# Optimization experiments

Hardware: AMD Instinct MI355X
Metric: run time of the kernel (lower is better)

Reference implementation:

```python
import jax, jax.numpy as jnp
import numpy as np

SEQ = 128; HID = 2048; NH = 8; NKV = 2; NREP = NH // NKV; HD = 256; FF = 4096
PLD = 256; NLT = 35; NLAYERS = 8; WIN = 512; FULL_LEN = 2048; PAST = 1024
FULL_LAYERS = {5}  # Gemma3 pattern: full attention when (i+1) % 6 == 0
PLE_PROJ_SCALE = HID ** -0.5
PLE_IN_SCALE = 0.7071067811865476  # rsqrt(2)
NEG = -1e9


def _rms(x, w, eps=1e-6):
    return x * jax.lax.rsqrt(jnp.mean(x * x, -1, keepdims=True) + eps) * w


def _vnorm(x, eps=1e-6):
    return x * jax.lax.rsqrt(jnp.mean(x * x, -1, keepdims=True) + eps)


def _rope(x, cos, sin):
    # x: (1, H, S, hd); cos/sin: (1, S, hd)
    c = cos[:, None]; s = sin[:, None]
    h = x.shape[-1] // 2
    x1, x2 = x[..., :h], x[..., h:]
    return x * c + jnp.concatenate([-x2, x1], -1) * s


def _rope_tables(pos, theta):
    inv = 1.0 / (theta ** (np.arange(0, HD, 2, dtype=np.float32) / HD))
    ang = pos[:, None] * inv[None, :]
    emb = np.concatenate([ang, ang], -1)  # (S, HD)
    return jnp.asarray(np.cos(emb), jnp.float32)[None], jnp.asarray(np.sin(emb), jnp.float32)[None]


def setup_inputs() -> dict:
    key = jax.random.key(0)
    ks = iter(jax.random.split(key, 64))
    f = lambda shape, s=0.02: jax.random.normal(next(ks), shape, dtype=jnp.float32) * s
    inp = {}
    inp['hidden_states'] = f((1, SEQ, HID), 1.0)
    inp['per_layer_raw'] = f((1, SEQ, NLT * PLD), 1.0)
    pos = np.arange(PAST, PAST + SEQ, dtype=np.float32)
    inp['cos_s'], inp['sin_s'] = _rope_tables(pos, 10000.0)
    inp['cos_f'], inp['sin_f'] = _rope_tables(pos, 1000000.0)
    i_s = np.arange(SEQ); j_f = np.arange(FULL_LEN); j_s = np.arange(WIN)
    inp['causal_mask_full'] = jnp.asarray(np.where(j_f[None, :] <= PAST + i_s[:, None], 0.0, NEG).astype(np.float32))[None, None]
    inp['causal_mask_sliding'] = jnp.asarray(np.where(j_s[None, :] <= WIN - SEQ + i_s[:, None], 0.0, NEG).astype(np.float32))[None, None]
    ind = np.zeros((FULL_LEN, SEQ), np.float32); ind[PAST + i_s, i_s] = 1.0
    inp['update_indicator'] = jnp.asarray(ind)[None, None]
    inp['K_sliding'] = f((7, NKV, WIN, HD), 1.0); inp['V_sliding'] = f((7, NKV, WIN, HD), 1.0)
    inp['K_full'] = f((1, NKV, FULL_LEN, HD), 1.0); inp['V_full'] = f((1, NKV, FULL_LEN, HD), 1.0)
    # learned parameters (stacked over the 8 layers)
    inp['Wq'] = f((NLAYERS, HID, NH * HD)); inp['Wk'] = f((NLAYERS, HID, NKV * HD))
    inp['Wv'] = f((NLAYERS, HID, NKV * HD)); inp['Wo'] = f((NLAYERS, NH * HD, HID))
    inp['w_in_ln'] = jnp.ones((NLAYERS, HID)); inp['w_q_norm'] = jnp.ones((NLAYERS, HD))
    inp['w_k_norm'] = jnp.ones((NLAYERS, HD)); inp['w_post_attn_ln'] = jnp.ones((NLAYERS, HID))
    inp['w_pre_ff_ln'] = jnp.ones((NLAYERS, HID))
    inp['Wgate'] = f((NLAYERS, HID, FF)); inp['Wup'] = f((NLAYERS, HID, FF)); inp['Wdown'] = f((NLAYERS, FF, HID))
    inp['w_post_ff_ln'] = jnp.ones((NLAYERS, HID))
    inp['Wple_gate'] = f((NLAYERS, HID, PLD)); inp['Wple_proj'] = f((NLAYERS, PLD, HID))
    inp['w_post_ple_ln'] = jnp.ones((NLAYERS, HID))
    inp['layer_scalar'] = jnp.ones((NLAYERS,))
    inp['Wple_model_proj'] = f((HID, NLT * PLD)); inp['w_ple_norm'] = jnp.ones((PLD,))
    return inp


def _forward(hidden_states, per_layer_raw, cos_s, sin_s, cos_f, sin_f,
             causal_mask_full, causal_mask_sliding, update_indicator,
             K_sliding, V_sliding, K_full, V_full,
             Wq, Wk, Wv, Wo, w_in_ln, w_q_norm, w_k_norm, w_post_attn_ln,
             w_pre_ff_ln, Wgate, Wup, Wdown, w_post_ff_ln,
             Wple_gate, Wple_proj, w_post_ple_ln, layer_scalar,
             Wple_model_proj, w_ple_norm):
    S = hidden_states.shape[1]
    # PLE: project hidden, per-layer RMSNorm over pld groups, combine with raw per-layer inputs
    proj = (hidden_states @ Wple_model_proj) * PLE_PROJ_SCALE  # (1,S,NLT*PLD)
    proj = _rms(proj.reshape(S, NLT, PLD), w_ple_norm)
    raw = per_layer_raw.reshape(S, NLT, PLD)
    ple = ((proj + raw) * PLE_IN_SCALE).reshape(1, S, NLT * PLD)

    hs = hidden_states
    Ks, Vs, Kf, Vf = K_sliding, V_sliding, K_full, V_full
    new_ks, new_vs = [], []
    si = 0; fi = 0
    for i in range(NLAYERS):
        is_full = i in FULL_LAYERS
        cos, sin = (cos_f, sin_f) if is_full else (cos_s, sin_s)
        res = hs
        h = _rms(hs, w_in_ln[i])
        # Q/K norm is per (token, head) RMS over head_dim, then RoPE
        q = _rms((h @ Wq[i]).reshape(1, S, NH, HD), w_q_norm[i]).transpose(0, 2, 1, 3)
        q = _rope(q, cos, sin)
        k = _rms((h @ Wk[i]).reshape(1, S, NKV, HD), w_k_norm[i]).transpose(0, 2, 1, 3)
        k = _rope(k, cos, sin)
        v = _vnorm((h @ Wv[i]).reshape(1, S, NKV, HD).transpose(0, 2, 1, 3))
        new_ks.append(k); new_vs.append(v)
        if is_full:
            # matmul-based indicator scatter into the full-attention cache slot
            k_sc = jnp.matmul(update_indicator, k)  # (1,NKV,FULL_LEN,HD)
            v_sc = jnp.matmul(update_indicator, v)
            cm = jnp.sum(update_indicator, -1, keepdims=True)  # (1,1,FULL_LEN,1)
            Kf = Kf.at[fi:fi + 1].set(Kf[fi:fi + 1] * (1.0 - cm) + k_sc)
            Vf = Vf.at[fi:fi + 1].set(Vf[fi:fi + 1] * (1.0 - cm) + v_sc)
            K_attn, V_attn, mask = Kf[fi:fi + 1], Vf[fi:fi + 1], causal_mask_full
            fi += 1
        else:
            # sliding-window shift: drop oldest S, append new K/V
            nk = jnp.concatenate([Ks[si:si + 1, :, S:, :], k], axis=2)
            nv = jnp.concatenate([Vs[si:si + 1, :, S:, :], v], axis=2)
            Ks = Ks.at[si:si + 1].set(nk); Vs = Vs.at[si:si + 1].set(nv)
            K_attn, V_attn, mask = nk, nv, causal_mask_sliding
            si += 1
        Ke = jnp.repeat(K_attn, NREP, axis=1)  # GQA repeat_interleave
        Ve = jnp.repeat(V_attn, NREP, axis=1)
        aw = jax.nn.softmax(jnp.einsum('bhsd,bhld->bhsl', q, Ke) + mask, axis=-1)  # no 1/sqrt(hd), as in source
        attn = jnp.einsum('bhsl,bhld->bhsd', aw, Ve).transpose(0, 2, 1, 3).reshape(1, S, NH * HD)
        hs = res + _rms(attn @ Wo[i], w_post_attn_ln[i])
        res = hs
        h2 = _rms(hs, w_pre_ff_ln[i])
        mlp = (jax.nn.gelu(h2 @ Wgate[i], approximate=True) * (h2 @ Wup[i])) @ Wdown[i]
        hs = res + _rms(mlp, w_post_ff_ln[i])
        res = hs
        pls = ple[:, :, i * PLD:(i + 1) * PLD]
        g = jax.nn.gelu(hs @ Wple_gate[i], approximate=True) * pls
        hs = res + _rms(g @ Wple_proj[i], w_post_ple_ln[i])
        hs = hs * layer_scalar[i]
    return hs, jnp.stack(new_ks), jnp.stack(new_vs)


def reference(hidden_states, per_layer_raw, cos_s, sin_s, cos_f, sin_f,
              causal_mask_full, causal_mask_sliding, update_indicator,
              K_sliding, V_sliding, K_full, V_full,
              Wq, Wk, Wv, Wo, w_in_ln, w_q_norm, w_k_norm, w_post_attn_ln,
              w_pre_ff_ln, Wgate, Wup, Wdown, w_post_ff_ln,
              Wple_gate, Wple_proj, w_post_ple_ln, layer_scalar,
              Wple_model_proj, w_ple_norm):
    return _forward(hidden_states, per_layer_raw, cos_s, sin_s, cos_f, sin_f,
                    causal_mask_full, causal_mask_sliding, update_indicator,
                    K_sliding, V_sliding, K_full, V_full,
                    Wq, Wk, Wv, Wo, w_in_ln, w_q_norm, w_k_norm, w_post_attn_ln,
                    w_pre_ff_ln, Wgate, Wup, Wdown, w_post_ff_ln,
                    Wple_gate, Wple_proj, w_post_ple_ln, layer_scalar,
                    Wple_model_proj, w_ple_norm)
```

## Files before the change

### kernel.cpp

```cpp
#include <hip/hip_runtime.h>
#include <stdint.h>

typedef short s16x8 __attribute__((ext_vector_type(8)));
typedef float f32x4 __attribute__((ext_vector_type(4)));
typedef unsigned short u16;

#define MFMA16(a,b,c) __builtin_amdgcn_mfma_f32_16x16x32_bf16((a),(b),(c),0,0,0)
#define ACAP 1184

__device__ __forceinline__ u16 f2bf(float f) {
  union { float f; unsigned u; } v; v.f = f;
  return (u16)((v.u + 0x7FFFu + ((v.u >> 16) & 1u)) >> 16);
}
__device__ __forceinline__ float bf2f(u16 u) {
  union { float f; unsigned v; } x; x.v = ((unsigned)u) << 16; return x.f;
}

__device__ __forceinline__ float block_sum256(float v, float* lred) {
  #pragma unroll
  for (int d = 32; d >= 1; d >>= 1) v += __shfl_xor(v, d);
  __syncthreads();
  if ((threadIdx.x & 63) == 0) lred[threadIdx.x >> 6] = v;
  __syncthreads();
  return (lred[0] + lred[1]) + (lred[2] + lred[3]);
}

__device__ __forceinline__ float gelu_t(float x) {
  float u = 0.7978845608028654f * (x + 0.044715f * x * x * x);
  return 0.5f * x * (1.0f + tanhf(u));
}

__global__ __launch_bounds__(256) void gemm3_k(
    const u16* __restrict__ Ah, const u16* __restrict__ Al, int lda,
    const float* __restrict__ W0, const float* __restrict__ W1, const float* __restrict__ W2,
    int e0, int e1, int ld0, int ld1, int ld2,
    float* __restrict__ out, int N, int kchunk, int Ktot)
{
  __shared__ float red[4 * 2048];
  const int n0 = blockIdx.x * 16;
  const int split = blockIdx.y;
  const float* W; int ldw, c0;
  if (n0 < e0)      { W = W0; ldw = ld0; c0 = n0; }
  else if (n0 < e1) { W = W1; ldw = ld1; c0 = n0 - e0; }
  else              { W = W2; ldw = ld2; c0 = n0 - e1; }
  const int w = threadIdx.x >> 6, l = threadIdx.x & 63;
  const int lr = l & 15, lh = l >> 4;
  const int wk = kchunk >> 2;
  const int k0 = split * kchunk + w * wk, k1 = k0 + wk;
  const u16* Abh = Ah + (size_t)lr * lda + 8 * lh;
  const u16* Abl = Al + (size_t)lr * lda + 8 * lh;
  const float* Wb = W + (size_t)(8 * lh) * ldw + (c0 + lr);

  f32x4 acc[8];
  #pragma unroll
  for (int i = 0; i < 8; i++) acc[i] = (f32x4){0.f,0.f,0.f,0.f};

  float bc[8];
  #pragma unroll
  for (int jj = 0; jj < 8; jj++) bc[jj] = Wb[(size_t)(k0 + jj) * ldw];

  for (int k = k0; k < k1; k += 32) {
    s16x8 ah[8], al[8];
    #pragma unroll
    for (int mt = 0; mt < 8; mt++) {
      ah[mt] = *(const s16x8*)(Abh + (size_t)(16*mt)*lda + k);
      al[mt] = *(const s16x8*)(Abl + (size_t)(16*mt)*lda + k);
    }
    float bn[8];
    if (k + 32 < k1) {
      #pragma unroll
      for (int jj = 0; jj < 8; jj++) bn[jj] = Wb[(size_t)(k + 32 + jj) * ldw];
    }
    s16x8 bh, bl;
    #pragma unroll
    for (int jj = 0; jj < 8; jj++) {
      union { float f; unsigned u; } wv; wv.f = bc[jj];
      bh[jj] = (short)(wv.u >> 16);
      union { float f; unsigned u; } hf; hf.u = wv.u & 0xFFFF0000u;
      union { float f; unsigned u; } lo; lo.f = wv.f - hf.f;
      bl[jj] = (short)(lo.u >> 16);
    }
    #pragma unroll
    for (int mt = 0; mt < 8; mt++) acc[mt] = MFMA16(ah[mt], bh, acc[mt]);
    #pragma unroll
    for (int mt = 0; mt < 8; mt++) acc[mt] = MFMA16(ah[mt], bl, acc[mt]);
    #pragma unroll
    for (int mt = 0; mt < 8; mt++) acc[mt] = MFMA16(al[mt], bh, acc[mt]);
    if (k + 32 < k1) {
      #pragma unroll
      for (int jj = 0; jj < 8; jj++) bc[jj] = bn[jj];
    }
  }
  #pragma unroll
  for (int mt = 0; mt < 8; mt++)
    #pragma unroll
    for (int r = 0; r < 4; r++)
      red[w * 2048 + (16*mt + 4*lh + r) * 16 + lr] = acc[mt][r];
  __syncthreads();
  const size_t ob = (size_t)split * (128 * (size_t)N) + n0;
  #pragma unroll
  for (int i = 0; i < 8; i++) {
    int e = threadIdx.x + 256 * i;
    int row = e >> 4, c = e & 15;
    float s = (red[e] + red[2048 + e]) + (red[4096 + e] + red[6144 + e]);
    out[ob + (size_t)row * N + c] = s;
  }
}

__global__ __launch_bounds__(256) void init_k(
    const float* __restrict__ hid, const float* __restrict__ w0,
    float* __restrict__ hs, u16* __restrict__ h0b, u16* __restrict__ h0l,
    u16* __restrict__ hbf, u16* __restrict__ hbl)
{
  __shared__ float lred[4];
  int s = blockIdx.x, t = threadIdx.x;
  float x[8]; float ss = 0.f;
  #pragma unroll
  for (int i = 0; i < 8; i++) {
    int j = t + 256 * i;
    float v = hid[(size_t)s * 2048 + j];
    x[i] = v; ss += v * v;
    hs[(size_t)s * 2048 + j] = v;
    u16 hi = f2bf(v);
    h0b[(size_t)s * 2048 + j] = hi;
    h0l[(size_t)s * 2048 + j] = f2bf(v - bf2f(hi));
  }
  ss = block_sum256(ss, lred);
  float rs = rsqrtf(ss * (1.f/2048.f) + 1e-6f);
  #pragma unroll
  for (int i = 0; i < 8; i++) {
    int j = t + 256 * i;
    float xn = x[i] * rs * w0[j];
    u16 hi = f2bf(xn);
    hbf[(size_t)s * 2048 + j] = hi;
    hbl[(size_t)s * 2048 + j] = f2bf(xn - bf2f(hi));
  }
}

__global__ __launch_bounds__(256) void ple_norm_k(
    const float* __restrict__ proj, const float* __restrict__ raw,
    const float* __restrict__ wp, float* __restrict__ ple)
{
  __shared__ float lred[4];
  int b = blockIdx.x;
  int s = b / 35, lt = b % 35, t = threadIdx.x;
  size_t idx = (size_t)s * 8960 + lt * 256 + t;
  float p = proj[idx] * 0.022097086912079612f;
  float ss = block_sum256(p * p, lred);
  float rs = rsqrtf(ss * (1.f/256.f) + 1e-6f);
  ple[idx] = (p * rs * wp[t] + raw[idx]) * 0.7071067811865476f;
}

__global__ __launch_bounds__(256) void fill_kv2_k(
    const float* __restrict__ oK, const float* __restrict__ oV,
    u16* __restrict__ Kh, u16* __restrict__ Kl,
    u16* __restrict__ VTh, u16* __restrict__ VTl,
    int olen, int ooff, int old_ld, int nA)
{
  __shared__ float tile[64][65];
  int b = blockIdx.x, t = threadIdx.x;
  if (b < nA) {
    size_t base = (size_t)b * 4096;
    #pragma unroll
    for (int i = 0; i < 16; i++) {
      size_t e = base + t + 256 * i;
      int kv = (int)(e / ((size_t)olen * 256));
      size_t rem = e - (size_t)kv * olen * 256;
      int j = (int)(rem >> 8), d = (int)(rem & 255);
      float v = oK[((size_t)kv * old_ld + ooff + j) * 256 + d];
      u16 hi = f2bf(v);
      size_t dst = (size_t)kv * (ACAP*256) + (size_t)j * 256 + d;
      Kh[dst] = hi;
      Kl[dst] = f2bf(v - bf2f(hi));
    }
  } else {
    int tb = b - nA;
    int tj = olen >> 6;
    int per_kv = tj * 4;
    int kv = tb / per_kv, rem = tb % per_kv;
    int j0 = (rem % tj) * 64, d0 = (rem / tj) * 64;
    #pragma unroll
    for (int i = 0; i < 16; i++) {
      int e = t + 256 * i;
      int jj = e >> 6, dd = e & 63;
      tile[jj][dd] = oV[((size_t)kv * old_ld + ooff + j0 + jj) * 256 + d0 + dd];
    }
    __syncthreads();
    #pragma unroll
    for (int i = 0; i < 16; i++) {
      int e = t + 256 * i;
      int dd = e >> 6, jj = e & 63;
      float v = tile[jj][dd];
      u16 hi = f2bf(v);
      size_t dst = (size_t)kv * (256*ACAP) + (size_t)(d0 + dd) * ACAP + (j0 + jj);
      VTh[dst] = hi;
      VTl[dst] = f2bf(v - bf2f(hi));
    }
  }
}

__global__ __launch_bounds__(256) void prep_attn_k(
    const float* __restrict__ qkvP, int nsplit,
    const float* __restrict__ wq, const float* __restrict__ wk,
    const float* __restrict__ cosb, const float* __restrict__ sinb,
    u16* __restrict__ qh, u16* __restrict__ ql,
    float* __restrict__ outk, float* __restrict__ outv,
    u16* __restrict__ Kh, u16* __restrict__ Kl,
    u16* __restrict__ VTh, u16* __restrict__ VTl, int jbase)
{
  __shared__ float lred[4];
  __shared__ float xs[256];
  int s = blockIdx.x, t = threadIdx.x;
  const float* base = qkvP + (size_t)s * 3072;
  float c = cosb[s * 256 + t], sn = sinb[s * 256 + t];
  #pragma unroll 1
  for (int h = 0; h < 8; h++) {
    float v = 0.f;
    for (int sp = 0; sp < nsplit; sp++) v += base[(size_t)sp * (128*3072) + h * 256 + t];
    float ss = block_sum256(v * v, lred);
    float rs = rsqrtf(ss * (1.f/256.f) + 1e-6f);
    float xn = v * rs * wq[t];
    xs[t] = xn;
    __syncthreads();
    float pr = xs[t ^ 128];
    float ro = (t < 128) ? -pr : pr;
    float qv = xn * c + ro * sn;
    u16 hi = f2bf(qv);
    qh[((size_t)h * 128 + s) * 256 + t] = hi;
    ql[((size_t)h * 128 + s) * 256 + t] = f2bf(qv - bf2f(hi));
    __syncthreads();
  }
  #pragma unroll 1
  for (int g = 0; g < 2; g++) {
    float v = 0.f;
    for (int sp = 0; sp < nsplit; sp++) v += base[(size_t)sp * (128*3072) + 2048 + g * 256 + t];
    float ss = block_sum256(v * v, lred);
    float rs = rsqrtf(ss * (1.f/256.f) + 1e-6f);
    float xn = v * rs * wk[t];
    xs[t] = xn;
    __syncthreads();
    float pr = xs[t ^ 128];
    float ro = (t < 128) ? -pr : pr;
    float kq = xn * c + ro * sn;
    outk[(size_t)g * (128*256) + s * 256 + t] = kq;
    u16 khi = f2bf(kq);
    size_t kdst = (size_t)g * (ACAP*256) + (size_t)(jbase + s) * 256 + t;
    Kh[kdst] = khi;
    Kl[kdst] = f2bf(kq - bf2f(khi));
    __syncthreads();
    float vv = 0.f;
    for (int sp = 0; sp < nsplit; sp++) vv += base[(size_t)sp * (128*3072) + 2560 + g * 256 + t];
    float ss2 = block_sum256(vv * vv, lred);
    float rs2 = rsqrtf(ss2 * (1.f/256.f) + 1e-6f);
    float vn = vv * rs2;
    outv[(size_t)g * (128*256) + s * 256 + t] = vn;
    u16 vhi = f2bf(vn);
    size_t vdst = (size_t)g * (256*ACAP) + (size_t)t * ACAP + (jbase + s);
    VTh[vdst] = vhi;
    VTl[vdst] = f2bf(vn - bf2f(vhi));
  }
}

__global__ __launch_bounds__(256) void attn6_k(
    const u16* __restrict__ qh, const u16* __restrict__ ql,
    const u16* __restrict__ Kh, const u16* __restrict__ Kl,
    const u16* __restrict__ VTh, const u16* __restrict__ VTl,
    float* __restrict__ Opart, float* __restrict__ ML, int off)
{
  __shared__ float OW[3][16][256];
  __shared__ float MW[4][16];
  __shared__ float LW[4][16];
  __shared__ u16 Ph[4][16*32];
  __shared__ u16 Pl[4][16*32];
  int bx = blockIdx.x;
  int ks = bx & 3;
  int b64 = bx >> 2;
  int h = b64 >> 3, qt = b64 & 7;
  int kv = h >> 2;
  int s0 = qt * 16;
  int nkeys = off + s0 + 16;
  int w = threadIdx.x >> 6, l = threadIdx.x & 63;
  int lr = l & 15, lh = l >> 4;
  int cw = ((nkeys + 511) >> 9) << 5;
  int g = ks * 4 + w;
  int jb = g * cw;
  int je = min(jb + cw, nkeys);
  const u16* Khb = Kh + (size_t)kv * (ACAP * 256);
  const u16* Klb = Kl + (size_t)kv * (ACAP * 256);
  const u16* Vhb = VTh + (size_t)kv * (256 * (size_t)ACAP);
  const u16* Vlb = VTl + (size_t)kv * (256 * (size_t)ACAP);

  s16x8 aqh[8], aql[8];
  {
    const u16* qrh = qh + ((size_t)h * 128 + s0 + lr) * 256 + 8 * lh;
    const u16* qrl = ql + ((size_t)h * 128 + s0 + lr) * 256 + 8 * lh;
    #pragma unroll
    for (int kk = 0; kk < 8; kk++) {
      aqh[kk] = *(const s16x8*)(qrh + kk * 32);
      aql[kk] = *(const s16x8*)(qrl + kk * 32);
    }
  }
  f32x4 accO[16];
  #pragma unroll
  for (int i = 0; i < 16; i++) accO[i] = (f32x4){0.f,0.f,0.f,0.f};
  float m_run[4], l_run[4];
  #pragma unroll
  for (int r = 0; r < 4; r++) { m_run[r] = -3.0e38f; l_run[r] = 0.f; }
  u16* Pwh = &Ph[w][0];
  u16* Pwl = &Pl[w][0];

  for (int j0 = jb; j0 < je; j0 += 32) {
    f32x4 lg[2];
    lg[0] = (f32x4){0.f,0.f,0.f,0.f};
    lg[1] = (f32x4){0.f,0.f,0.f,0.f};
    #pragma unroll
    for (int kk = 0; kk < 8; kk++) {
      const u16* kb0 = Khb + (size_t)(j0 + lr) * 256 + kk * 32 + 8 * lh;
      const u16* kb1 = Khb + (size_t)(j0 + 16 + lr) * 256 + kk * 32 + 8 * lh;
      const u16* kl0 = Klb + (size_t)(j0 + lr) * 256 + kk * 32 + 8 * lh;
      const u16* kl1 = Klb + (size_t)(j0 + 16 + lr) * 256 + kk * 32 + 8 * lh;
      s16x8 b0h = *(const s16x8*)kb0, b1h = *(const s16x8*)kb1;
      s16x8 b0l = *(const s16x8*)kl0, b1l = *(const s16x8*)kl1;
      lg[0] = MFMA16(aqh[kk], b0h, lg[0]);
      lg[1] = MFMA16(aqh[kk], b1h, lg[1]);
      lg[0] = MFMA16(aqh[kk], b0l, lg[0]);
      lg[1] = MFMA16(aqh[kk], b1l, lg[1]);
      lg[0] = MFMA16(aql[kk], b0h, lg[0]);
      lg[1] = MFMA16(aql[kk], b1h, lg[1]);
    }
    float tmax[4];
    #pragma unroll
    for (int r = 0; r < 4; r++) tmax[r] = -1.0e30f;
    #pragma unroll
    for (int tt = 0; tt < 2; tt++) {
      int j = j0 + 16 * tt + lr;
      #pragma unroll
      for (int r = 0; r < 4; r++)
        if (j <= off + s0 + 4 * lh + r) tmax[r] = fmaxf(tmax[r], lg[tt][r]);
    }
    #pragma unroll
    for (int d = 1; d < 16; d <<= 1)
      #pragma unroll
      for (int r = 0; r < 4; r++) tmax[r] = fmaxf(tmax[r], __shfl_xor(tmax[r], d));
    float scl[4], rsum[4];
    #pragma unroll
    for (int r = 0; r < 4; r++) {
      float mn = fmaxf(m_run[r], tmax[r]);
      scl[r] = __expf(m_run[r] - mn);
      m_run[r] = mn;
      rsum[r] = 0.f;
    }
    #pragma unroll
    for (int tt = 0; tt < 2; tt++) {
      int j = j0 + 16 * tt + lr;
      #pragma unroll
      for (int r = 0; r < 4; r++) {
        bool valid = (j <= off + s0 + 4 * lh + r);
        float p = valid ? __expf(lg[tt][r] - m_run[r]) : 0.f;
        lg[tt][r] = p;
        rsum[r] += p;
      }
    }
    #pragma unroll
    for (int d = 1; d < 16; d <<= 1)
      #pragma unroll
      for (int r = 0; r < 4; r++) rsum[r] += __shfl_xor(rsum[r], d);
    #pragma unroll
    for (int r = 0; r < 4; r++) l_run[r] = l_run[r] * scl[r] + rsum[r];
    #pragma unroll
    for (int tt = 0; tt < 2; tt++) {
      #pragma unroll
      for (int r = 0; r < 4; r++) {
        float p = lg[tt][r];
        u16 phi = f2bf(p);
        Pwh[(4 * lh + r) * 32 + 16 * tt + lr] = phi;
        Pwl[(4 * lh + r) * 32 + 16 * tt + lr] = f2bf(p - bf2f(phi));
      }
    }
    #pragma unroll
    for (int t2 = 0; t2 < 16; t2++)
      #pragma unroll
      for (int r = 0; r < 4; r++) accO[t2][r] *= scl[r];
    s16x8 pah = *(const s16x8*)(Pwh + lr * 32 + 8 * lh);
    s16x8 pal = *(const s16x8*)(Pwl + lr * 32 + 8 * lh);
    #pragma unroll
    for (int t2 = 0; t2 < 16; t2++) {
      s16x8 bvh = *(const s16x8*)(Vhb + (size_t)(16 * t2 + lr) * ACAP + j0 + 8 * lh);
      s16x8 bvl = *(const s16x8*)(Vlb + (size_t)(16 * t2 + lr) * ACAP + j0 + 8 * lh);
      accO[t2] = MFMA16(pah, bvh, accO[t2]);
      accO[t2] = MFMA16(pah, bvl, accO[t2]);
      accO[t2] = MFMA16(pal, bvh, accO[t2]);
    }
  }
  if (w > 0) {
    #pragma unroll
    for (int t2 = 0; t2 < 16; t2++)
      #pragma unroll
      for (int r = 0; r < 4; r++)
        OW[w - 1][4 * lh + r][16 * t2 + lr] = accO[t2][r];
  }
  if (lr == 0) {
    #pragma unroll
    for (int r = 0; r < 4; r++) { MW[w][4 * lh + r] = m_run[r]; LW[w][4 * lh + r] = l_run[r]; }
  }
  __syncthreads();
  if (w == 0) {
    float ew[4][4];
    float Mrow[4], Lrow[4];
    #pragma unroll
    for (int r = 0; r < 4; r++) {
      int row = 4 * lh + r;
      float M = fmaxf(fmaxf(m_run[r], MW[1][row]), fmaxf(MW[2][row], MW[3][row]));
      ew[r][0] = __expf(m_run[r] - M);
      ew[r][1] = __expf(MW[1][row] - M);
      ew[r][2] = __expf(MW[2][row] - M);
      ew[r][3] = __expf(MW[3][row] - M);
      Lrow[r] = l_run[r] * ew[r][0] + LW[1][row] * ew[r][1] + LW[2][row] * ew[r][2] + LW[3][row] * ew[r][3];
      Mrow[r] = M;
    }
    float* Ob = Opart + (size_t)bx * 4096;
    #pragma unroll
    for (int t2 = 0; t2 < 16; t2++) {
      #pragma unroll
      for (int r = 0; r < 4; r++) {
        int row = 4 * lh + r, c = 16 * t2 + lr;
        float o = accO[t2][r] * ew[r][0] + OW[0][row][c] * ew[r][1]
                + OW[1][row][c] * ew[r][2] + OW[2][row][c] * ew[r][3];
        Ob[row * 256 + c] = o;
      }
    }
    if (lr == 0) {
      #pragma unroll
      for (int r = 0; r < 4; r++) {
        int row = 4 * lh + r;
        ML[bx * 32 + row] = Mrow[r];
        ML[bx * 32 + 16 + row] = Lrow[r];
      }
    }
  }
}

__global__ __launch_bounds__(256) void attn_comb_k(
    const float* __restrict__ Opart, const float* __restrict__ ML,
    u16* __restrict__ outbf, u16* __restrict__ outlo)
{
  int b = blockIdx.x;
  int h = b >> 3, qt = b & 7, s0 = qt * 16;
  int c = threadIdx.x;
  #pragma unroll 1
  for (int row = 0; row < 16; row++) {
    float m[4], lv[4];
    #pragma unroll
    for (int ks = 0; ks < 4; ks++) {
      m[ks]  = ML[(b * 4 + ks) * 32 + row];
      lv[ks] = ML[(b * 4 + ks) * 32 + 16 + row];
    }
    float Mg = fmaxf(fmaxf(m[0], m[1]), fmaxf(m[2], m[3]));
    float L = 0.f, o = 0.f;
    #pragma unroll
    for (int ks = 0; ks < 4; ks++) {
      float e = __expf(m[ks] - Mg);
      L += lv[ks] * e;
      o += Opart[((size_t)(b * 4 + ks)) * 4096 + row * 256 + c] * e;
    }
    float val = o / L;
    u16 hi = f2bf(val);
    outbf[(size_t)(s0 + row) * 2048 + h * 256 + c] = hi;
    outlo[(size_t)(s0 + row) * 2048 + h * 256 + c] = f2bf(val - bf2f(hi));
  }
}

__global__ __launch_bounds__(256) void norm_res_k(
    const float* __restrict__ parts, int nsplit,
    const float* __restrict__ wn, float* __restrict__ hs,
    const float* __restrict__ w2, u16* __restrict__ outbf, u16* __restrict__ outlo,
    const float* __restrict__ scp, float* __restrict__ outf)
{
  __shared__ float lred[4];
  int row = blockIdx.x, t = threadIdx.x;
  const float* pr = parts + (size_t)row * 2048;
  float x[8]; float ss = 0.f;
  #pragma unroll
  for (int i = 0; i < 8; i++) {
    int j = t + 256 * i;
    float v = 0.f;
    for (int sp = 0; sp < nsplit; sp++) v += pr[(size_t)sp * (128*2048) + j];
    x[i] = v; ss += v * v;
  }
  ss = block_sum256(ss, lred);
  float rs = rsqrtf(ss * (1.f/2048.f) + 1e-6f);
  float sc = scp ? scp[0] : 1.f;
  float y[8]; float ss2 = 0.f;
  #pragma unroll
  for (int i = 0; i < 8; i++) {
    int j = t + 256 * i;
    float v = (hs[(size_t)row * 2048 + j] + x[i] * rs * wn[j]) * sc;
    y[i] = v; ss2 += v * v;
    hs[(size_t)row * 2048 + j] = v;
    if (outf) outf[(size_t)row * 2048 + j] = v;
  }
  if (outbf) {
    if (w2) {
      ss2 = block_sum256(ss2, lred);
      float rs2 = rsqrtf(ss2 * (1.f/2048.f) + 1e-6f);
      #pragma unroll
      for (int i = 0; i < 8; i++) {
        int j = t + 256 * i;
        float xn = y[i] * rs2 * w2[j];
        u16 hi = f2bf(xn);
        outbf[(size_t)row * 2048 + j] = hi;
        if (outlo) outlo[(size_t)row * 2048 + j] = f2bf(xn - bf2f(hi));
      }
    } else {
      #pragma unroll
      for (int i = 0; i < 8; i++) {
        int j = t + 256 * i;
        u16 hi = f2bf(y[i]);
        outbf[(size_t)row * 2048 + j] = hi;
        if (outlo) outlo[(size_t)row * 2048 + j] = f2bf(y[i] - bf2f(hi));
      }
    }
  }
}

__global__ __launch_bounds__(256) void mlp_act_k(
    const float* __restrict__ gu, int nsplit, u16* __restrict__ out, u16* __restrict__ outlo)
{
  int base = blockIdx.x * 1024 + threadIdx.x * 4;
  int row = base >> 12, j = base & 4095;
  float g[4] = {0,0,0,0}, u[4] = {0,0,0,0};
  for (int sp = 0; sp < nsplit; sp++) {
    const float4 gg = *(const float4*)(gu + (size_t)sp * (128*8192) + (size_t)row * 8192 + j);
    const float4 uu = *(const float4*)(gu + (size_t)sp * (128*8192) + (size_t)row * 8192 + 4096 + j);
    g[0]+=gg.x; g[1]+=gg.y; g[2]+=gg.z; g[3]+=gg.w;
    u[0]+=uu.x; u[1]+=uu.y; u[2]+=uu.z; u[3]+=uu.w;
  }
  size_t ob = (size_t)row * 4096 + j;
  #pragma unroll
  for (int q = 0; q < 4; q++) {
    float val = gelu_t(g[q]) * u[q];
    u16 hi = f2bf(val);
    out[ob + q] = hi;
    outlo[ob + q] = f2bf(val - bf2f(hi));
  }
}

__global__ __launch_bounds__(256) void ple_act_k(
    const float* __restrict__ pgP, int nsplit, const float* __restrict__ ple,
    int layer, u16* __restrict__ gbf, u16* __restrict__ gbl)
{
  int s = blockIdx.x, t = threadIdx.x;
  float x = 0.f;
  for (int sp = 0; sp < nsplit; sp++) x += pgP[(size_t)sp * (128*256) + s * 256 + t];
  float val = gelu_t(x) * ple[(size_t)s * 8960 + layer * 256 + t];
  u16 hi = f2bf(val);
  gbf[s * 256 + t] = hi;
  gbl[s * 256 + t] = f2bf(val - bf2f(hi));
}

extern "C" void kernel_launch(void* const* d_in, const int* in_sizes, int n_in,
                              void* d_out, int out_size, void* d_ws, size_t ws_size,
                              hipStream_t stream)
{
  const float* hid   = (const float*)d_in[0];
  const float* raw   = (const float*)d_in[1];
  const float* cos_s = (const float*)d_in[2];
  const float* sin_s = (const float*)d_in[3];
  const float* cos_f = (const float*)d_in[4];
  const float* sin_f = (const float*)d_in[5];
  const float* Ksl   = (const float*)d_in[9];
  const float* Vsl   = (const float*)d_in[10];
  const float* Kfu   = (const float*)d_in[11];
  const float* Vfu   = (const float*)d_in[12];
  const float* Wq    = (const float*)d_in[13];
  const float* Wk    = (const float*)d_in[14];
  const float* Wv    = (const float*)d_in[15];
  const float* Wo    = (const float*)d_in[16];
  const float* w_in  = (const float*)d_in[17];
  const float* w_qn  = (const float*)d_in[18];
  const float* w_kn  = (const float*)d_in[19];
  const float* w_pa  = (const float*)d_in[20];
  const float* w_pf  = (const float*)d_in[21];
  const float* Wg    = (const float*)d_in[22];
  const float* Wu    = (const float*)d_in[23];
  const float* Wd    = (const float*)d_in[24];
  const float* w_ff  = (const float*)d_in[25];
  const float* Wpg   = (const float*)d_in[26];
  const float* Wpp   = (const float*)d_in[27];
  const float* w_pp  = (const float*)d_in[28];
  const float* lsc   = (const float*)d_in[29];
  const float* Wpm   = (const float*)d_in[30];
  const float* w_pn  = (const float*)d_in[31];

  char* ws = (char*)d_ws;
  size_t off = 0;
  auto alloc = [&](size_t b) { size_t o = off; off += (b + 255) & ~(size_t)255; return o; };
  size_t o_hs   = alloc(128*2048*4);
  size_t o_qkvP = alloc(4ull*128*3072*4);
  size_t o_t1P  = alloc(4ull*128*2048*4);
  size_t o_guP  = alloc(2ull*128*8192*4);
  size_t o_t2P  = alloc(4ull*128*2048*4);
  size_t o_pgP  = alloc(8ull*128*256*4);
  size_t o_t3P  = alloc(2ull*128*2048*4);
  size_t o_ple  = alloc(128ull*8960*4);
  size_t o_h0b  = alloc(128*2048*2);
  size_t o_h0l  = alloc(128*2048*2);
  size_t o_hb   = alloc(128*2048*2);
  size_t o_hbl  = alloc(128*2048*2);
  size_t o_h2b  = alloc(128*2048*2);
  size_t o_h2l  = alloc(128*2048*2);
  size_t o_hrb  = alloc(128*2048*2);
  size_t o_hrl  = alloc(128*2048*2);
  size_t o_ab   = alloc(128*2048*2);
  size_t o_abl  = alloc(128*2048*2);
  size_t o_mb   = alloc(128ull*4096*2);
  size_t o_mbl  = alloc(128ull*4096*2);
  size_t o_gb   = alloc(128*256*2);
  size_t o_gbl  = alloc(128*256*2);
  size_t o_qh   = alloc(8ull*128*256*2);
  size_t o_ql   = alloc(8ull*128*256*2);
  size_t o_Kh   = alloc(2ull*ACAP*256*2);
  size_t o_Kl   = alloc(2ull*ACAP*256*2);
  size_t o_VTh  = alloc(2ull*256*ACAP*2);
  size_t o_VTl  = alloc(2ull*256*ACAP*2);
  size_t o_Op   = alloc(256ull*4096*4);
  size_t o_ML   = alloc(256ull*32*4);

  float* hs   = (float*)(ws + o_hs);
  float* qkvP = (float*)(ws + o_qkvP);
  float* t1P  = (float*)(ws + o_t1P);
  float* guP  = (float*)(ws + o_guP);
  float* t2P  = (float*)(ws + o_t2P);
  float* pgP  = (float*)(ws + o_pgP);
  float* t3P  = (float*)(ws + o_t3P);
  float* ple  = (float*)(ws + o_ple);
  float* proj = (float*)(ws + o_qkvP);
  u16* h0b = (u16*)(ws + o_h0b);
  u16* h0l = (u16*)(ws + o_h0l);
  u16* hb  = (u16*)(ws + o_hb);
  u16* hbl = (u16*)(ws + o_hbl);
  u16* h2b = (u16*)(ws + o_h2b);
  u16* h2l = (u16*)(ws + o_h2l);
  u16* hrb = (u16*)(ws + o_hrb);
  u16* hrl = (u16*)(ws + o_hrl);
  u16* ab  = (u16*)(ws + o_ab);
  u16* abl = (u16*)(ws + o_abl);
  u16* mb  = (u16*)(ws + o_mb);
  u16* mbl = (u16*)(ws + o_mbl);
  u16* gb  = (u16*)(ws + o_gb);
  u16* gbl = (u16*)(ws + o_gbl);
  u16* qhb = (u16*)(ws + o_qh);
  u16* qlb = (u16*)(ws + o_ql);
  u16* Khc = (u16*)(ws + o_Kh);
  u16* Klc = (u16*)(ws + o_Kl);
  u16* VThc = (u16*)(ws + o_VTh);
  u16* VTlc = (u16*)(ws + o_VTl);
  float* Opart = (float*)(ws + o_Op);
  float* MLb   = (float*)(ws + o_ML);

  float* ouths = (float*)d_out;
  float* outk  = ouths + 128*2048;
  float* outv  = outk + 8*2*128*256;

  init_k<<<128, 256, 0, stream>>>(hid, w_in, hs, h0b, h0l, hb, hbl);
  gemm3_k<<<dim3(560,1), 256, 0, stream>>>(h0b, h0l, 2048, Wpm, Wpm, Wpm,
      8960, 8960, 8960, 8960, 8960, proj, 8960, 2048, 2048);
  ple_norm_k<<<128*35, 256, 0, stream>>>(proj, raw, w_pn, ple);

  for (int i = 0; i < 8; i++) {
    bool full = (i == 5);
    int si = (i < 5) ? i : i - 1;
    const float* cs = full ? cos_f : cos_s;
    const float* sn = full ? sin_f : sin_s;
    int jbase = full ? 1024 : 384;
    if (full) {
      fill_kv2_k<<<256, 256, 0, stream>>>(Kfu, Vfu, Khc, Klc, VThc, VTlc, 1024, 0, 2048, 128);
    } else {
      fill_kv2_k<<<96, 256, 0, stream>>>(Ksl + (size_t)si*2*512*256, Vsl + (size_t)si*2*512*256,
                                         Khc, Klc, VThc, VTlc, 384, 128, 512, 48);
    }
    gemm3_k<<<dim3(192,4), 256, 0, stream>>>(hb, hbl, 2048,
        Wq + (size_t)i*2048*2048, Wk + (size_t)i*2048*512, Wv + (size_t)i*2048*512,
        2048, 2560, 2048, 512, 512, qkvP, 3072, 512, 2048);
    prep_attn_k<<<128, 256, 0, stream>>>(qkvP, 4, w_qn + i*256, w_kn + i*256, cs, sn,
        qhb, qlb, outk + (size_t)i*65536, outv + (size_t)i*65536, Khc, Klc, VThc, VTlc, jbase);
    attn6_k<<<256, 256, 0, stream>>>(qhb, qlb, Khc, Klc, VThc, VTlc, Opart, MLb, jbase);
    attn_comb_k<<<64, 256, 0, stream>>>(Opart, MLb, ab, abl);
    gemm3_k<<<dim3(128,4), 256, 0, stream>>>(ab, abl, 2048,
        Wo + (size_t)i*2048*2048, Wo, Wo, 2048, 2048, 2048, 2048, 2048,
        t1P, 2048, 512, 2048);
    norm_res_k<<<128, 256, 0, stream>>>(t1P, 4, w_pa + i*2048, hs,
        w_pf + i*2048, h2b, h2l, nullptr, nullptr);
    gemm3_k<<<dim3(512,2), 256, 0, stream>>>(h2b, h2l, 2048,
        Wg + (size_t)i*2048*4096, Wu + (size_t)i*2048*4096, Wu,
        4096, 8192, 4096, 4096, 4096, guP, 8192, 1024, 2048);
    mlp_act_k<<<512, 256, 0, stream>>>(guP, 2, mb, mbl);
    gemm3_k<<<dim3(128,4), 256, 0, stream>>>(mb, mbl, 4096,
        Wd + (size_t)i*4096*2048, Wd, Wd, 2048, 2048, 2048, 2048, 2048,
        t2P, 2048, 1024, 4096);
    norm_res_k<<<128, 256, 0, stream>>>(t2P, 4, w_ff + i*2048, hs,
        nullptr, hrb, hrl, nullptr, nullptr);
    gemm3_k<<<dim3(16,8), 256, 0, stream>>>(hrb, hrl, 2048,
        Wpg + (size_t)i*2048*256, Wpg, Wpg, 256, 256, 256, 256, 256,
        pgP, 256, 256, 2048);
    ple_act_k<<<128, 256, 0, stream>>>(pgP, 8, ple, i, gb, gbl);
    gemm3_k<<<dim3(128,2), 256, 0, stream>>>(gb, gbl, 256,
        Wpp + (size_t)i*256*2048, Wpp, Wpp, 2048, 2048, 2048, 2048, 2048,
        t3P, 2048, 128, 256);
    norm_res_k<<<128, 256, 0, stream>>>(t3P, 2, w_pp + i*2048, hs,
        (i < 7) ? (w_in + (i+1)*2048) : nullptr,
        (i < 7) ? hb : nullptr,
        (i < 7) ? hbl : nullptr,
        lsc + i, (i == 7) ? ouths : nullptr);
  }
}
```

Before: 2.354 ms.

## Give each wave its own N tile and move split-K reduction to consumers

The GEMM kernel now assigns each of the four waves a separate 16-column tile over the full block K chunk, instead of splitting K across waves and reducing through shared memory. Each wave writes its partial result straight to global memory. The split-K factor rises, so downstream kernels sum more partials. A-operand loads are also software-pipelined one step ahead. The change removes the LDS reduction and barrier, and each block now covers 64 columns. In exchange there is more partial-sum traffic and a larger workspace, and the A tile is no longer shared between waves.

Measured after the change: 3.125 ms. +32.8%, slower.

```diff
diff --git a/kernel.cpp b/kernel.cpp
--- a/kernel.cpp
+++ b/kernel.cpp
@@ -30,23 +30,20 @@
   return 0.5f * x * (1.0f + tanhf(u));
 }
 
-__global__ __launch_bounds__(256) void gemm3_k(
+__global__ __launch_bounds__(256) void gemm4_k(
     const u16* __restrict__ Ah, const u16* __restrict__ Al, int lda,
     const float* __restrict__ W0, const float* __restrict__ W1, const float* __restrict__ W2,
     int e0, int e1, int ld0, int ld1, int ld2,
-    float* __restrict__ out, int N, int kchunk, int Ktot)
-{
-  __shared__ float red[4 * 2048];
-  const int n0 = blockIdx.x * 16;
-  const int split = blockIdx.y;
+    float* __restrict__ out, int N, int kchunk)
+{
+  const int w = threadIdx.x >> 6, l = threadIdx.x & 63;
+  const int lr = l & 15, lh = l >> 4;
+  const int n0 = blockIdx.x * 64 + w * 16;
   const float* W; int ldw, c0;
   if (n0 < e0)      { W = W0; ldw = ld0; c0 = n0; }
   else if (n0 < e1) { W = W1; ldw = ld1; c0 = n0 - e0; }
   else              { W = W2; ldw = ld2; c0 = n0 - e1; }
-  const int w = threadIdx.x >> 6, l = threadIdx.x & 63;
-  const int lr = l & 15, lh = l >> 4;
-  const int wk = kchunk >> 2;
-  const int k0 = split * kchunk + w * wk, k1 = k0 + wk;
+  const int k0 = blockIdx.y * kchunk, k1 = k0 + kchunk;
   const u16* Abh = Ah + (size_t)lr * lda + 8 * lh;
   const u16* Abl = Al + (size_t)lr * lda + 8 * lh;
   const float* Wb = W + (size_t)(8 * lh) * ldw + (c0 + lr);
@@ -55,19 +52,23 @@
   #pragma unroll
   for (int i = 0; i < 8; i++) acc[i] = (f32x4){0.f,0.f,0.f,0.f};
 
-  float bc[8];
+  s16x8 ah[8], al[8]; float bc[8];
+  #pragma unroll
+  for (int mt = 0; mt < 8; mt++) {
+    ah[mt] = *(const s16x8*)(Abh + (size_t)(16*mt)*lda + k0);
+    al[mt] = *(const s16x8*)(Abl + (size_t)(16*mt)*lda + k0);
+  }
   #pragma unroll
   for (int jj = 0; jj < 8; jj++) bc[jj] = Wb[(size_t)(k0 + jj) * ldw];
 
   for (int k = k0; k < k1; k += 32) {
-    s16x8 ah[8], al[8];
-    #pragma unroll
-    for (int mt = 0; mt < 8; mt++) {
-      ah[mt] = *(const s16x8*)(Abh + (size_t)(16*mt)*lda + k);
-      al[mt] = *(const s16x8*)(Abl + (size_t)(16*mt)*lda + k);
-    }
-    float bn[8];
+    s16x8 anh[8], anl[8]; float bn[8];
     if (k + 32 < k1) {
+      #pragma unroll
+      for (int mt = 0; mt < 8; mt++) {
+        anh[mt] = *(const s16x8*)(Abh + (size_t)(16*mt)*lda + k + 32);
+        anl[mt] = *(const s16x8*)(Abl + (size_t)(16*mt)*lda + k + 32);
+      }
       #pragma unroll
       for (int jj = 0; jj < 8; jj++) bn[jj] = Wb[(size_t)(k + 32 + jj) * ldw];
     }
@@ -88,23 +89,17 @@
     for (int mt = 0; mt < 8; mt++) acc[mt] = MFMA16(al[mt], bh, acc[mt]);
     if (k + 32 < k1) {
       #pragma unroll
+      for (int mt = 0; mt < 8; mt++) { ah[mt] = anh[mt]; al[mt] = anl[mt]; }
+      #pragma unroll
       for (int jj = 0; jj < 8; jj++) bc[jj] = bn[jj];
     }
   }
+  const size_t ob = (size_t)blockIdx.y * (128 * (size_t)N);
   #pragma unroll
   for (int mt = 0; mt < 8; mt++)
     #pragma unroll
     for (int r = 0; r < 4; r++)
-      red[w * 2048 + (16*mt + 4*lh + r) * 16 + lr] = acc[mt][r];
-  __syncthreads();
-  const size_t ob = (size_t)split * (128 * (size_t)N) + n0;
-  #pragma unroll
-  for (int i = 0; i < 8; i++) {
-    int e = threadIdx.x + 256 * i;
-    int row = e >> 4, c = e & 15;
-    float s = (red[e] + red[2048 + e]) + (red[4096 + e] + red[6144 + e]);
-    out[ob + (size_t)row * N + c] = s;
-  }
+      out[ob + (size_t)(16*mt + 4*lh + r) * N + n0 + lr] = acc[mt][r];
 }
 
 __global__ __launch_bounds__(256) void init_k(
@@ -138,14 +133,16 @@
 }
 
 __global__ __launch_bounds__(256) void ple_norm_k(
-    const float* __restrict__ proj, const float* __restrict__ raw,
+    const float* __restrict__ proj, int nsplit, const float* __restrict__ raw,
     const float* __restrict__ wp, float* __restrict__ ple)
 {
   __shared__ float lred[4];
   int b = blockIdx.x;
   int s = b / 35, lt = b % 35, t = threadIdx.x;
   size_t idx = (size_t)s * 8960 + lt * 256 + t;
-  float p = proj[idx] * 0.022097086912079612f;
+  float p = 0.f;
+  for (int sp = 0; sp < nsplit; sp++) p += proj[(size_t)sp * (128*8960) + idx];
+  p *= 0.022097086912079612f;
   float ss = block_sum256(p * p, lred);
   float rs = rsqrtf(ss * (1.f/256.f) + 1e-6f);
   ple[idx] = (p * rs * wp[t] + raw[idx]) * 0.7071067811865476f;
@@ -596,13 +593,14 @@
   size_t off = 0;
   auto alloc = [&](size_t b) { size_t o = off; off += (b + 255) & ~(size_t)255; return o; };
   size_t o_hs   = alloc(128*2048*4);
-  size_t o_qkvP = alloc(4ull*128*3072*4);
-  size_t o_t1P  = alloc(4ull*128*2048*4);
-  size_t o_guP  = alloc(2ull*128*8192*4);
-  size_t o_t2P  = alloc(4ull*128*2048*4);
-  size_t o_pgP  = alloc(8ull*128*256*4);
-  size_t o_t3P  = alloc(2ull*128*2048*4);
+  size_t o_qkvP = alloc(16ull*128*3072*4);
+  size_t o_t1P  = alloc(16ull*128*2048*4);
+  size_t o_guP  = alloc(4ull*128*8192*4);
+  size_t o_t2P  = alloc(16ull*128*2048*4);
+  size_t o_pgP  = alloc(32ull*128*256*4);
+  size_t o_t3P  = alloc(8ull*128*2048*4);
   size_t o_ple  = alloc(128ull*8960*4);
+  size_t o_proj = alloc(4ull*128*8960*4);
   size_t o_h0b  = alloc(128*2048*2);
   size_t o_h0l  = alloc(128*2048*2);
   size_t o_hb   = alloc(128*2048*2);
@@ -634,7 +632,7 @@
   float* pgP  = (float*)(ws + o_pgP);
   float* t3P  = (float*)(ws + o_t3P);
   float* ple  = (float*)(ws + o_ple);
-  float* proj = (float*)(ws + o_qkvP);
+  float* proj = (float*)(ws + o_proj);
   u16* h0b = (u16*)(ws + o_h0b);
   u16* h0l = (u16*)(ws + o_h0l);
   u16* hb  = (u16*)(ws + o_hb);
@@ -663,9 +661,9 @@
   float* outv  = outk + 8*2*128*256;
 
   init_k<<<128, 256, 0, stream>>>(hid, w_in, hs, h0b, h0l, hb, hbl);
-  gemm3_k<<<dim3(560,1), 256, 0, stream>>>(h0b, h0l, 2048, Wpm, Wpm, Wpm,
-      8960, 8960, 8960, 8960, 8960, proj, 8960, 2048, 2048);
-  ple_norm_k<<<128*35, 256, 0, stream>>>(proj, raw, w_pn, ple);
+  gemm4_k<<<dim3(140,4), 256, 0, stream>>>(h0b, h0l, 2048, Wpm, Wpm, Wpm,
+      8960, 8960, 8960, 8960, 8960, proj, 8960, 512);
+  ple_norm_k<<<128*35, 256, 0, stream>>>(proj, 4, raw, w_pn, ple);
 
   for (int i = 0; i < 8; i++) {
     bool full = (i == 5);
@@ -679,35 +677,35 @@
       fill_kv2_k<<<96, 256, 0, stream>>>(Ksl + (size_t)si*2*512*256, Vsl + (size_t)si*2*512*256,
                                          Khc, Klc, VThc, VTlc, 384, 128, 512, 48);
     }
-    gemm3_k<<<dim3(192,4), 256, 0, stream>>>(hb, hbl, 2048,
+    gemm4_k<<<dim3(48,16), 256, 0, stream>>>(hb, hbl, 2048,
         Wq + (size_t)i*2048*2048, Wk + (size_t)i*2048*512, Wv + (size_t)i*2048*512,
-        2048, 2560, 2048, 512, 512, qkvP, 3072, 512, 2048);
-    prep_attn_k<<<128, 256, 0, stream>>>(qkvP, 4, w_qn + i*256, w_kn + i*256, cs, sn,
+        2048, 2560, 2048, 512, 512, qkvP, 3072, 128);
+    prep_attn_k<<<128, 256, 0, stream>>>(qkvP, 16, w_qn + i*256, w_kn + i*256, cs, sn,
         qhb, qlb, outk + (size_t)i*65536, outv + (size_t)i*65536, Khc, Klc, VThc, VTlc, jbase);
     attn6_k<<<256, 256, 0, stream>>>(qhb, qlb, Khc, Klc, VThc, VTlc, Opart, MLb, jbase);
     attn_comb_k<<<64, 256, 0, stream>>>(Opart, MLb, ab, abl);
-    gemm3_k<<<dim3(128,4), 256, 0, stream>>>(ab, abl, 2048,
+    gemm4_k<<<dim3(32,16), 256, 0, stream>>>(ab, abl, 2048,
         Wo + (size_t)i*2048*2048, Wo, Wo, 2048, 2048, 2048, 2048, 2048,
-        t1P, 2048, 512, 2048);
-    norm_res_k<<<128, 256, 0, stream>>>(t1P, 4, w_pa + i*2048, hs,
+        t1P, 2048, 128);
+    norm_res_k<<<128, 256, 0, stream>>>(t1P, 16, w_pa + i*2048, hs,
         w_pf + i*2048, h2b, h2l, nullptr, nullptr);
-    gemm3_k<<<dim3(512,2), 256, 0, stream>>>(h2b, h2l, 2048,
+    gemm4_k<<<dim3(128,4), 256, 0, stream>>>(h2b, h2l, 2048,
         Wg + (size_t)i*2048*4096, Wu + (size_t)i*2048*4096, Wu,
-        4096, 8192, 4096, 4096, 4096, guP, 8192, 1024, 2048);
-    mlp_act_k<<<512, 256, 0, stream>>>(guP, 2, mb, mbl);
-    gemm3_k<<<dim3(128,4), 256, 0, stream>>>(mb, mbl, 4096,
+        4096, 8192, 4096, 4096, 4096, guP, 8192, 512);
+    mlp_act_k<<<512, 256, 0, stream>>>(guP, 4, mb, mbl);
+    gemm4_k<<<dim3(32,16), 256, 0, stream>>>(mb, mbl, 4096,
         Wd + (size_t)i*4096*2048, Wd, Wd, 2048, 2048, 2048, 2048, 2048,
-        t2P, 2048, 1024, 4096);
-    norm_res_k<<<128, 256, 0, stream>>>(t2P, 4, w_ff + i*2048, hs,
+        t2P, 2048, 256);
+    norm_res_k<<<128, 256, 0, stream>>>(t2P, 16, w_ff + i*2048, hs,
         nullptr, hrb, hrl, nullptr, nullptr);
-    gemm3_k<<<dim3(16,8), 256, 0, stream>>>(hrb, hrl, 2048,
+    gemm4_k<<<dim3(4,32), 256, 0, stream>>>(hrb, hrl, 2048,
         Wpg + (size_t)i*2048*256, Wpg, Wpg, 256, 256, 256, 256, 256,
-        pgP, 256, 256, 2048);
-    ple_act_k<<<128, 256, 0, stream>>>(pgP, 8, ple, i, gb, gbl);
-    gemm3_k<<<dim3(128,2), 256, 0, stream>>>(gb, gbl, 256,
+        pgP, 256, 64);
+    ple_act_k<<<128, 256, 0, stream>>>(pgP, 32, ple, i, gb, gbl);
+    gemm4_k<<<dim3(32,8), 256, 0, stream>>>(gb, gbl, 256,
         Wpp + (size_t)i*256*2048, Wpp, Wpp, 2048, 2048, 2048, 2048, 2048,
-        t3P, 2048, 128, 256);
-    norm_res_k<<<128, 256, 0, stream>>>(t3P, 2, w_pp + i*2048, hs,
+        t3P, 2048, 32);
+    norm_res_k<<<128, 256, 0, stream>>>(t3P, 8, w_pp + i*2048, hs,
         (i < 7) ? (w_in + (i+1)*2048) : nullptr,
         (i < 7) ? hb : nullptr,
         (i < 7) ? hbl : nullptr,
```
